# Performance work log

Hardware: AMD Instinct MI355X
Metric: run time of the kernel (lower is better)

Reference implementation:

```python
import jax, jax.numpy as jnp
import numpy as np

B, S, DIN, PPOS = 2, 128, 768, 256
DCAT = 2 * (DIN + PPOS)   # 2048, BiLSTM input dim
H = DCAT // 2             # 1024, LSTM hidden per direction
MAXLEN = 128              # position embedding table size


def _xavier(k, shape):
    lim = float(np.sqrt(6.0 / (shape[0] + shape[1])))
    return jax.random.uniform(k, shape, jnp.float32, -lim, lim)


def _lstm_u(k, shape):
    lim = float(1.0 / np.sqrt(H))
    return jax.random.uniform(k, shape, jnp.float32, -lim, lim)


def setup_inputs() -> dict:
    key = jax.random.key(0)
    ks = jax.random.split(key, 17)
    inp = {
        "input_embeddings": jax.random.normal(ks[0], (B, S, DIN), jnp.float32),
        "pos_emb": _xavier(ks[1], (MAXLEN, PPOS)),
    }
    i = 2
    for l in (0, 1):
        for d in ("f", "b"):
            inp[f"w_ih_l{l}_{d}"] = _lstm_u(ks[i], (4 * H, DCAT)); i += 1
            inp[f"b_ih_l{l}_{d}"] = _lstm_u(ks[i], (4 * H,)); i += 1
            inp[f"b_hh_l{l}_{d}"] = _lstm_u(ks[i], (4 * H,)); i += 1
    inp["fc_w"] = _lstm_u(ks[i], (1, 2 * H)); i += 1
    inp["fc_b"] = _lstm_u(ks[i], (1,))
    inp["convo_len"] = S
    return inp


def _lstm_dir(x, w_ih, b_ih, b_hh):
    # single timestep, h0=c0=0 -> recurrent term vanishes (grad wrt W_hh is 0)
    g = x @ w_ih.T + b_ih + b_hh            # [N, 4H], pytorch gate order i,f,g,o
    i, f, c, o = jnp.split(g, 4, axis=-1)
    cell = jax.nn.sigmoid(i) * jnp.tanh(c)  # f-gate multiplies c0=0
    return jax.nn.sigmoid(o) * jnp.tanh(cell)


def reference(input_embeddings, pos_emb,
              w_ih_l0_f, b_ih_l0_f, b_hh_l0_f,
              w_ih_l0_b, b_ih_l0_b, b_hh_l0_b,
              w_ih_l1_f, b_ih_l1_f, b_hh_l1_f,
              w_ih_l1_b, b_ih_l1_b, b_hh_l1_b,
              fc_w, fc_b, convo_len):
    # positions indexed by int(norm(embedding)) as in the original code
    idx = jnp.linalg.norm(input_embeddings, axis=-1).astype(jnp.int32)  # [B,S]
    e = jnp.concatenate([input_embeddings, pos_emb[idx]], axis=-1)      # [B,S,D']
    # pair (i,j) -> concat(e_i, e_j)
    left = jnp.repeat(e, S, axis=1)          # [B, S*S, D'], row i repeated S times
    right = jnp.tile(e, (1, S, 1))           # [B, S*S, D'], sequence tiled S times
    p = jnp.concatenate([left, right], axis=-1).reshape(B * S * S, DCAT)
    h1 = jnp.concatenate([
        _lstm_dir(p, w_ih_l0_f, b_ih_l0_f, b_hh_l0_f),
        _lstm_dir(p, w_ih_l0_b, b_ih_l0_b, b_hh_l0_b)], axis=-1)        # [N, 2H]
    h2 = jnp.concatenate([
        _lstm_dir(h1, w_ih_l1_f, b_ih_l1_f, b_hh_l1_f),
        _lstm_dir(h1, w_ih_l1_b, b_ih_l1_b, b_hh_l1_b)], axis=-1)       # [N, 2H]
    logits = h2 @ fc_w.T + fc_b              # [N, 1]
    return logits.reshape(B, S * S)
```

## Files before the change

kernel.cpp:

```cpp
#include <hip/hip_runtime.h>
#include <cstdint>

typedef _Float16 f16;
typedef f16   f16x8 __attribute__((ext_vector_type(8)));
typedef f16   f16x4 __attribute__((ext_vector_type(4)));
typedef float f32x4 __attribute__((ext_vector_type(4)));
typedef float f32x8 __attribute__((ext_vector_type(8)));
typedef int   i32x4 __attribute__((ext_vector_type(4)));
typedef signed char c8x8 __attribute__((ext_vector_type(8)));
typedef unsigned int u32;


static constexpr size_t OFF_E16  = 0;
static constexpr size_t OFF_W0P  = 524288;
static constexpr size_t OFF_UV   = 34078720;
static constexpr size_t OFF_B0   = 50855936;
static constexpr size_t OFF_W1P  = 50888704;
static constexpr size_t OFF_B1   = 76054528;
static constexpr size_t OFF_H1   = 76079104;
static constexpr size_t OFF_PART = 210296832;

__device__ __forceinline__ void gl_lds16(const void* g, void* l) {
  __builtin_amdgcn_global_load_lds((const __attribute__((address_space(1))) u32*)g,
                                   (__attribute__((address_space(3))) u32*)l, 16, 0, 0);
}
__device__ __forceinline__ float sigm(float x) { return 1.f / (1.f + __expf(-x)); }
__device__ __forceinline__ float tanh_f(float x) {
  float e = __expf(-2.f * fabsf(x));
  float t = (1.f - e) / (1.f + e);
  return x < 0.f ? -t : t;
}


__global__ __launch_bounds__(256) void prep_e(const float* __restrict__ x,
                                              const float* __restrict__ pos,
                                              f16* __restrict__ e16) {
  int row = blockIdx.x;
  const float* xr = x + (size_t)row * 768;
  double ss = 0.0;
  for (int i = threadIdx.x; i < 768; i += 256) { float v = xr[i]; ss += (double)v * v; }
  __shared__ double red[256];
  red[threadIdx.x] = ss;
  __syncthreads();
  for (int s2 = 128; s2 > 0; s2 >>= 1) {
    if (threadIdx.x < s2) red[threadIdx.x] += red[threadIdx.x + s2];
    __syncthreads();
  }
  __shared__ int idx_s;
  if (threadIdx.x == 0) {
    int idx = (int)((float)sqrt(red[0]));
    idx_s = idx < 0 ? 0 : (idx > 127 ? 127 : idx);
  }
  __syncthreads();
  int idx = idx_s;
  for (int i = threadIdx.x; i < 1024; i += 256) {
    float v = (i < 768) ? xr[i] : pos[idx * 256 + (i - 768)];
    e16[(size_t)row * 1024 + i] = (f16)v;
  }
}

__global__ __launch_bounds__(256) void prep_w0(const float* __restrict__ w0f,
                                               const float* __restrict__ w0b,
                                               f16* __restrict__ w0p) {
  int t = blockIdx.x * 256 + threadIdx.x;
  int n = t >> 8;
  int k4 = (t & 255) * 4;
  int half = n >> 13;
  int nn = n & 8191;
  int d = nn >> 12;
  int r = nn & 4095;
  const float* w = d ? w0b : w0f;
  float4 v = *(const float4*)(w + (size_t)r * 2048 + half * 1024 + k4);
  f16x4 o;
  o[0] = (f16)v.x; o[1] = (f16)v.y; o[2] = (f16)v.z; o[3] = (f16)v.w;
  *(f16x4*)(w0p + (size_t)n * 1024 + k4) = o;
}

__global__ __launch_bounds__(256) void prep_w1(const float* __restrict__ w1f,
                                               const float* __restrict__ w1b,
                                               signed char* __restrict__ w1q) {
  int t = blockIdx.x * 256 + threadIdx.x;
  int n = t >> 8;
  int c8 = (t & 255) * 8;
  int ct = n / 192, r = n % 192;
  int wn = r / 48, r2 = r % 48;
  int g = r2 >> 4, hs = r2 & 15;
  int d = ct >> 4;
  int h = (ct & 15) * 64 + wn * 16 + hs;
  int gsel = (g == 0) ? 0 : (g + 1);
  const float* w = d ? w1b : w1f;
  const float* src = w + (size_t)(gsel * 1024 + h) * 2048 + c8;
  float4 v0 = *(const float4*)(src);
  float4 v1 = *(const float4*)(src + 4);
  c8x8 o;
  o[0] = (signed char)(int)rintf(v0.x * 4064.f);
  o[1] = (signed char)(int)rintf(v0.y * 4064.f);
  o[2] = (signed char)(int)rintf(v0.z * 4064.f);
  o[3] = (signed char)(int)rintf(v0.w * 4064.f);
  o[4] = (signed char)(int)rintf(v1.x * 4064.f);
  o[5] = (signed char)(int)rintf(v1.y * 4064.f);
  o[6] = (signed char)(int)rintf(v1.z * 4064.f);
  o[7] = (signed char)(int)rintf(v1.w * 4064.f);
  *(c8x8*)(w1q + (size_t)n * 2048 + c8) = o;
}

__global__ void prep_bias(const float* bi0f, const float* bh0f,
                          const float* bi0b, const float* bh0b,
                          const float* bi1f, const float* bh1f,
                          const float* bi1b, const float* bh1b,
                          float* bias0, float* bias1) {
  int i = blockIdx.x * 256 + threadIdx.x;
  if (i < 8192) {
    int d = i >> 12, r = i & 4095;
    bias0[i] = d ? (bi0b[r] + bh0b[r]) : (bi0f[r] + bh0f[r]);
  } else if (i < 8192 + 6144) {
    int n = i - 8192;
    int d = n / 3072, rem = n % 3072;
    int g3 = rem >> 10, k = rem & 1023;
    int gsel = (g3 == 0) ? 0 : (g3 + 1);
    int r = gsel * 1024 + k;
    bias1[n] = d ? (bi1b[r] + bh1b[r]) : (bi1f[r] + bh1f[r]);
  }
}

__global__ __launch_bounds__(256) void gemm_l0(const f16* __restrict__ e16,
                                               const f16* __restrict__ w0p,
                                               float* __restrict__ uv) {
  __shared__ __align__(16) f16 As[8192];
  __shared__ __align__(16) f16 Bs[8192];
  int n0 = blockIdx.x * 128;
  int m0 = blockIdx.y * 128;
  int tid = threadIdx.x, lane = tid & 63, w = tid >> 6;
  int wr = (w >> 1) * 64, wc = (w & 1) * 64;
  f32x4 acc[4][4] = {};

  for (int k0 = 0; k0 < 1024; k0 += 64) {
    __syncthreads();
#pragma unroll
    for (int q = 0; q < 4; q++) {
      int ch = tid + q * 256;
      int c = ch >> 7, r = ch & 127;
      gl_lds16(e16 + (size_t)(m0 + r) * 1024 + k0 + c * 8, (char*)As + ch * 16);
    }
#pragma unroll
    for (int q = 0; q < 4; q++) {
      int ch = tid + q * 256;
      int c = ch >> 7, r = ch & 127;
      gl_lds16(w0p + (size_t)(n0 + r) * 1024 + k0 + c * 8, (char*)Bs + ch * 16);
    }
    __syncthreads();
#pragma unroll
    for (int ks = 0; ks < 2; ks++) {
      int cb = ks * 4 + (lane >> 4);
      f16x8 a[4], b[4];
#pragma unroll
      for (int f = 0; f < 4; f++)
        a[f] = *(const f16x8*)(As + (cb * 128 + wr + f * 16 + (lane & 15)) * 8);
#pragma unroll
      for (int g = 0; g < 4; g++)
        b[g] = *(const f16x8*)(Bs + (cb * 128 + wc + g * 16 + (lane & 15)) * 8);
#pragma unroll
      for (int f = 0; f < 4; f++)
#pragma unroll
        for (int g = 0; g < 4; g++)
          acc[f][g] = __builtin_amdgcn_mfma_f32_16x16x32_f16(a[f], b[g], acc[f][g], 0, 0, 0);
    }
  }
  int col = lane & 15, lg = lane >> 4;
#pragma unroll
  for (int f = 0; f < 4; f++)
#pragma unroll
    for (int g = 0; g < 4; g++)
#pragma unroll
      for (int j = 0; j < 4; j++) {
        int row = m0 + wr + f * 16 + lg * 4 + j;
        int c = n0 + wc + g * 16 + col;
        uv[(size_t)row * 16384 + c] = acc[f][g][j];
      }
}

__global__ __launch_bounds__(256) void pair_h1(const float* __restrict__ uv,
                                               const float* __restrict__ bias0,
                                               signed char* __restrict__ h1q) {
  int row = blockIdx.x;
  int urow = row >> 7;
  int b = row >> 14;
  int vrow = (b << 7) | (row & 127);
  int t = threadIdx.x;
  int u = t * 8;
  int d = u >> 10, k = u & 1023;
  const float* ub = uv + (size_t)urow * 16384 + d * 4096 + k;
  const float* vb = uv + (size_t)vrow * 16384 + 8192 + d * 4096 + k;
  const float* bb = bias0 + d * 4096 + k;
  f32x8 ui = *(const f32x8*)(ub);
  f32x8 uc = *(const f32x8*)(ub + 2048);
  f32x8 uo = *(const f32x8*)(ub + 3072);
  f32x8 vi = *(const f32x8*)(vb);
  f32x8 vc = *(const f32x8*)(vb + 2048);
  f32x8 vo = *(const f32x8*)(vb + 3072);
  f32x8 bi = *(const f32x8*)(bb);
  f32x8 bc = *(const f32x8*)(bb + 2048);
  f32x8 bo = *(const f32x8*)(bb + 3072);
  c8x8 ov;
#pragma unroll
  for (int e = 0; e < 8; e++) {
    float gi = ui[e] + vi[e] + bi[e];
    float gc = uc[e] + vc[e] + bc[e];
    float go = uo[e] + vo[e] + bo[e];
    float cell = sigm(gi) * tanh_f(gc);
    float hv = sigm(go) * tanh_f(cell);
    ov[e] = (signed char)(int)rintf(hv * 127.f);
  }
  *(c8x8*)(h1q + (size_t)row * 2048 + u) = ov;
}

__global__ __launch_bounds__(256, 2) void gemm_l1(const signed char* __restrict__ h1q,
                                                  const signed char* __restrict__ w1q,
                                                  const float* __restrict__ bias1,
                                                  const float* __restrict__ fcw,
                                                  float* __restrict__ partial) {
  __shared__ __align__(16) signed char As[2][16384];
  __shared__ __align__(16) signed char Bs[2][24576];
  int ct = blockIdx.x;
  int m0 = blockIdx.y * 128;
  int d = ct >> 4;
  int tid = threadIdx.x, lane = tid & 63;
  int wn = tid >> 6;
  int la = lane & 15, lq = lane >> 4, l8 = lane & 7;

  const signed char* asrc[4]; signed char* adst[4];
#pragma unroll
  for (int q = 0; q < 4; q++) {
    int ch = tid + q * 256, r = ch >> 3, slot = ch & 7, c = slot ^ (r & 7);
    asrc[q] = h1q + (size_t)(m0 + r) * 2048 + c * 16;
    adst[q] = &As[0][ch * 16];
  }
  const signed char* bsrc[6]; signed char* bdst[6];
#pragma unroll
  for (int q = 0; q < 6; q++) {
    int ch = tid + q * 256, pr = ch >> 3, slot = ch & 7, c = slot ^ (pr & 7);
    bsrc[q] = w1q + (size_t)(ct * 192 + pr) * 2048 + c * 16;
    bdst[q] = &Bs[0][ch * 16];
  }
  auto stage = [&](int t, int b) {
#pragma unroll
    for (int q = 0; q < 4; q++) gl_lds16(asrc[q] + t * 128, adst[q] + b * 16384);
#pragma unroll
    for (int q = 0; q < 6; q++) gl_lds16(bsrc[q] + t * 128, bdst[q] + b * 24576);
  };

  i32x4 acc[8][3] = {};
  stage(0, 0);
  stage(1, 1);
  asm volatile("s_waitcnt vmcnt(10)" ::: "memory");
  __builtin_amdgcn_s_barrier();

  for (int t = 0; t < 16; ++t) {
    int b = t & 1;
    const signed char* Ab = &As[b][0];
    const signed char* Bb = &Bs[b][0];
    i32x4 af[2][8], bf[2][3];
#pragma unroll
    for (int ks = 0; ks < 2; ks++) {
      int slot = (ks * 4 + lq) ^ l8;
#pragma unroll
      for (int rf = 0; rf < 8; rf++)
        af[ks][rf] = *(const i32x4*)(Ab + ((rf * 16 + la) * 8 + slot) * 16);
#pragma unroll
      for (int cf = 0; cf < 3; cf++)
        bf[ks][cf] = *(const i32x4*)(Bb + ((wn * 48 + cf * 16 + la) * 8 + slot) * 16);
    }
    __builtin_amdgcn_s_setprio(1);
#pragma unroll
    for (int rf = 0; rf < 8; rf++)
#pragma unroll
      for (int cf = 0; cf < 3; cf++)
        acc[rf][cf] = __builtin_amdgcn_mfma_i32_16x16x64_i8(af[0][rf], bf[0][cf], acc[rf][cf], 0, 0, 0);
    __builtin_amdgcn_s_setprio(0);
    asm volatile("s_waitcnt lgkmcnt(0)" ::: "memory");
    __builtin_amdgcn_sched_barrier(0);
    __builtin_amdgcn_s_barrier();
    if (t < 14) stage(t + 2, b);
    __builtin_amdgcn_s_setprio(1);
#pragma unroll
    for (int rf = 0; rf < 8; rf++)
#pragma unroll
      for (int cf = 0; cf < 3; cf++)
        acc[rf][cf] = __builtin_amdgcn_mfma_i32_16x16x64_i8(af[1][rf], bf[1][cf], acc[rf][cf], 0, 0, 0);
    __builtin_amdgcn_s_setprio(0);
    if (t < 14)      { asm volatile("s_waitcnt vmcnt(10)" ::: "memory"); }
    else if (t == 14){ asm volatile("s_waitcnt vmcnt(0)"  ::: "memory"); }
    __builtin_amdgcn_s_barrier();
  }

  float* sred = (float*)&As[0][0];
  const float S = 1.0f / 516128.0f;
  int hcol = (ct & 15) * 64 + wn * 16 + la;
  float bi = bias1[(d * 3 + 0) * 1024 + hcol];
  float bc = bias1[(d * 3 + 1) * 1024 + hcol];
  float bo = bias1[(d * 3 + 2) * 1024 + hcol];
  float wf = fcw[d * 1024 + hcol];
#pragma unroll
  for (int rf = 0; rf < 8; rf++) {
#pragma unroll
    for (int j = 0; j < 4; j++) {
      float gi = (float)acc[rf][0][j] * S + bi;
      float gc = (float)acc[rf][1][j] * S + bc;
      float go = (float)acc[rf][2][j] * S + bo;
      float cell = sigm(gi) * tanh_f(gc);
      float hv = sigm(go) * tanh_f(cell);
      float v = hv * wf;
      v += __shfl_xor(v, 1);
      v += __shfl_xor(v, 2);
      v += __shfl_xor(v, 4);
      v += __shfl_xor(v, 8);
      if (la == 0) sred[wn * 128 + rf * 16 + lq * 4 + j] = v;
    }
  }
  __syncthreads();
  if (tid < 128) {
    float s = sred[tid] + sred[128 + tid] + sred[256 + tid] + sred[384 + tid];
    partial[(size_t)ct * 32768 + m0 + tid] = s;
  }
}

__global__ void reduce_out(const float* __restrict__ partial,
                           const float* __restrict__ fcb,
                           float* __restrict__ out) {
  int m = blockIdx.x * 256 + threadIdx.x;
  float s = fcb[0];
#pragma unroll
  for (int ct = 0; ct < 32; ct++) s += partial[(size_t)ct * 32768 + m];
  out[m] = s;
}

extern "C" void kernel_launch(void* const* d_in, const int* in_sizes, int n_in,
                              void* d_out, int out_size, void* d_ws, size_t ws_size,
                              hipStream_t stream) {
  const float* x    = (const float*)d_in[0];
  const float* pos  = (const float*)d_in[1];
  const float* w0f  = (const float*)d_in[2];
  const float* bi0f = (const float*)d_in[3];
  const float* bh0f = (const float*)d_in[4];
  const float* w0b  = (const float*)d_in[5];
  const float* bi0b = (const float*)d_in[6];
  const float* bh0b = (const float*)d_in[7];
  const float* w1f  = (const float*)d_in[8];
  const float* bi1f = (const float*)d_in[9];
  const float* bh1f = (const float*)d_in[10];
  const float* w1b  = (const float*)d_in[11];
  const float* bi1b = (const float*)d_in[12];
  const float* bh1b = (const float*)d_in[13];
  const float* fcw  = (const float*)d_in[14];
  const float* fcb  = (const float*)d_in[15];
  float* out = (float*)d_out;

  char* ws = (char*)d_ws;
  f16*   e16   = (f16*)(ws + OFF_E16);
  f16*   w0p   = (f16*)(ws + OFF_W0P);
  float* uv    = (float*)(ws + OFF_UV);
  float* bias0 = (float*)(ws + OFF_B0);
  signed char* w1q = (signed char*)(ws + OFF_W1P);
  float* bias1 = (float*)(ws + OFF_B1);
  signed char* h1q = (signed char*)(ws + OFF_H1);
  float* part  = (float*)(ws + OFF_PART);

  prep_e<<<256, 256, 0, stream>>>(x, pos, e16);
  prep_w0<<<16384, 256, 0, stream>>>(w0f, w0b, w0p);
  prep_w1<<<6144, 256, 0, stream>>>(w1f, w1b, w1q);
  prep_bias<<<56, 256, 0, stream>>>(bi0f, bh0f, bi0b, bh0b, bi1f, bh1f, bi1b, bh1b,
                                    bias0, bias1);
  gemm_l0<<<dim3(128, 2), 256, 0, stream>>>(e16, w0p, uv);
  pair_h1<<<32768, 256, 0, stream>>>(uv, bias0, h1q);
  gemm_l1<<<dim3(32, 256), 256, 0, stream>>>(h1q, w1q, bias1, fcw, part);
  reduce_out<<<128, 256, 0, stream>>>(part, fcb, out);
}
```

Before: 722.2 us.

## Enlarge layer-1 GEMM tile to 256 rows with 8 waves and interleaved staging

The int8 layer-1 GEMM block now covers 256 rows by 192 weight columns using 512 threads arranged as 2x4 waves, so each weight tile loaded into LDS serves twice as many rows. The K loop is split into four sub-phases, and the next tile's A and B global-to-LDS copies are issued during the first two, in a double-buffered pipeline. The grid is reordered so consecutive blocks share the same weight column tile. The cost is more barriers per K step, a larger LDS footprint (112KB per block) and possibly lower occupancy.

Result: slower. 795.0 us (+10.1%).

```diff
diff --git a/kernel.cpp b/kernel.cpp
--- a/kernel.cpp
+++ b/kernel.cpp
@@ -214,83 +214,92 @@
   *(c8x8*)(h1q + (size_t)row * 2048 + u) = ov;
 }
 
-__global__ __launch_bounds__(256, 2) void gemm_l1(const signed char* __restrict__ h1q,
+__global__ __launch_bounds__(512, 2) void gemm_l1(const signed char* __restrict__ h1q,
                                                   const signed char* __restrict__ w1q,
                                                   const float* __restrict__ bias1,
                                                   const float* __restrict__ fcw,
                                                   float* __restrict__ partial) {
-  __shared__ __align__(16) signed char As[2][16384];
+  __shared__ __align__(16) signed char As[2][32768];
   __shared__ __align__(16) signed char Bs[2][24576];
-  int ct = blockIdx.x;
-  int m0 = blockIdx.y * 128;
+  int m0 = blockIdx.x * 256;
+  int ct = blockIdx.y;
   int d = ct >> 4;
-  int tid = threadIdx.x, lane = tid & 63;
-  int wn = tid >> 6;
+  int tid = threadIdx.x, lane = tid & 63, w = tid >> 6;
+  int wm = w >> 2, wn = w & 3;
   int la = lane & 15, lq = lane >> 4, l8 = lane & 7;
 
   const signed char* asrc[4]; signed char* adst[4];
 #pragma unroll
   for (int q = 0; q < 4; q++) {
-    int ch = tid + q * 256, r = ch >> 3, slot = ch & 7, c = slot ^ (r & 7);
+    int ch = tid + q * 512, r = ch >> 3, slot = ch & 7, c = slot ^ (r & 7);
     asrc[q] = h1q + (size_t)(m0 + r) * 2048 + c * 16;
     adst[q] = &As[0][ch * 16];
   }
-  const signed char* bsrc[6]; signed char* bdst[6];
-#pragma unroll
-  for (int q = 0; q < 6; q++) {
-    int ch = tid + q * 256, pr = ch >> 3, slot = ch & 7, c = slot ^ (pr & 7);
+  const signed char* bsrc[3]; signed char* bdst[3];
+#pragma unroll
+  for (int q = 0; q < 3; q++) {
+    int ch = tid + q * 512, pr = ch >> 3, slot = ch & 7, c = slot ^ (pr & 7);
     bsrc[q] = w1q + (size_t)(ct * 192 + pr) * 2048 + c * 16;
     bdst[q] = &Bs[0][ch * 16];
   }
-  auto stage = [&](int t, int b) {
-#pragma unroll
-    for (int q = 0; q < 4; q++) gl_lds16(asrc[q] + t * 128, adst[q] + b * 16384);
-#pragma unroll
-    for (int q = 0; q < 6; q++) gl_lds16(bsrc[q] + t * 128, bdst[q] + b * 24576);
+  auto stageA = [&](int t, int b) {
+#pragma unroll
+    for (int q = 0; q < 4; q++) gl_lds16(asrc[q] + t * 128, adst[q] + b * 32768);
   };
+  auto stageB = [&](int t, int b) {
+#pragma unroll
+    for (int q = 0; q < 3; q++) gl_lds16(bsrc[q] + t * 128, bdst[q] + b * 24576);
+  };
 
   i32x4 acc[8][3] = {};
-  stage(0, 0);
-  stage(1, 1);
-  asm volatile("s_waitcnt vmcnt(10)" ::: "memory");
+  stageA(0, 0); stageB(0, 0);
+  asm volatile("s_waitcnt vmcnt(0)" ::: "memory");
   __builtin_amdgcn_s_barrier();
 
   for (int t = 0; t < 16; ++t) {
     int b = t & 1;
     const signed char* Ab = &As[b][0];
     const signed char* Bb = &Bs[b][0];
-    i32x4 af[2][8], bf[2][3];
-#pragma unroll
-    for (int ks = 0; ks < 2; ks++) {
-      int slot = (ks * 4 + lq) ^ l8;
-#pragma unroll
-      for (int rf = 0; rf < 8; rf++)
-        af[ks][rf] = *(const i32x4*)(Ab + ((rf * 16 + la) * 8 + slot) * 16);
-#pragma unroll
-      for (int cf = 0; cf < 3; cf++)
-        bf[ks][cf] = *(const i32x4*)(Bb + ((wn * 48 + cf * 16 + la) * 8 + slot) * 16);
-    }
-    __builtin_amdgcn_s_setprio(1);
-#pragma unroll
-    for (int rf = 0; rf < 8; rf++)
-#pragma unroll
-      for (int cf = 0; cf < 3; cf++)
-        acc[rf][cf] = __builtin_amdgcn_mfma_i32_16x16x64_i8(af[0][rf], bf[0][cf], acc[rf][cf], 0, 0, 0);
-    __builtin_amdgcn_s_setprio(0);
-    asm volatile("s_waitcnt lgkmcnt(0)" ::: "memory");
-    __builtin_amdgcn_sched_barrier(0);
-    __builtin_amdgcn_s_barrier();
-    if (t < 14) stage(t + 2, b);
-    __builtin_amdgcn_s_setprio(1);
-#pragma unroll
-    for (int rf = 0; rf < 8; rf++)
-#pragma unroll
-      for (int cf = 0; cf < 3; cf++)
-        acc[rf][cf] = __builtin_amdgcn_mfma_i32_16x16x64_i8(af[1][rf], bf[1][cf], acc[rf][cf], 0, 0, 0);
-    __builtin_amdgcn_s_setprio(0);
-    if (t < 14)      { asm volatile("s_waitcnt vmcnt(10)" ::: "memory"); }
-    else if (t == 14){ asm volatile("s_waitcnt vmcnt(0)"  ::: "memory"); }
-    __builtin_amdgcn_s_barrier();
+    i32x4 bf[2][3];
+#pragma unroll
+    for (int p = 0; p < 4; p++) {
+      i32x4 a[2][2];
+#pragma unroll
+      for (int ks = 0; ks < 2; ks++) {
+        int slot = (ks * 4 + lq) ^ l8;
+#pragma unroll
+        for (int rq = 0; rq < 2; rq++) {
+          int R = wm * 128 + (p * 2 + rq) * 16 + la;
+          a[ks][rq] = *(const i32x4*)(Ab + (R * 8 + slot) * 16);
+        }
+        if (p == 0) {
+#pragma unroll
+          for (int cf = 0; cf < 3; cf++) {
+            int P = wn * 48 + cf * 16 + la;
+            bf[ks][cf] = *(const i32x4*)(Bb + (P * 8 + slot) * 16);
+          }
+        }
+      }
+      if (t < 15) {
+        if (p == 0) stageA(t + 1, b ^ 1);
+        else if (p == 1) stageB(t + 1, b ^ 1);
+      }
+      __builtin_amdgcn_s_barrier();
+      asm volatile("s_waitcnt lgkmcnt(0)" ::: "memory");
+      __builtin_amdgcn_sched_barrier(0);
+      __builtin_amdgcn_s_setprio(1);
+#pragma unroll
+      for (int ks = 0; ks < 2; ks++)
+#pragma unroll
+        for (int rq = 0; rq < 2; rq++)
+#pragma unroll
+          for (int cf = 0; cf < 3; cf++)
+            acc[p * 2 + rq][cf] = __builtin_amdgcn_mfma_i32_16x16x64_i8(
+                a[ks][rq], bf[ks][cf], acc[p * 2 + rq][cf], 0, 0, 0);
+      __builtin_amdgcn_s_setprio(0);
+      if (p == 3 && t < 15) { asm volatile("s_waitcnt vmcnt(0)" ::: "memory"); }
+      __builtin_amdgcn_s_barrier();
+    }
   }
 
   float* sred = (float*)&As[0][0];
@@ -314,12 +323,12 @@
       v += __shfl_xor(v, 2);
       v += __shfl_xor(v, 4);
       v += __shfl_xor(v, 8);
-      if (la == 0) sred[wn * 128 + rf * 16 + lq * 4 + j] = v;
+      if (la == 0) sred[wn * 256 + wm * 128 + rf * 16 + lq * 4 + j] = v;
     }
   }
   __syncthreads();
-  if (tid < 128) {
-    float s = sred[tid] + sred[128 + tid] + sred[256 + tid] + sred[384 + tid];
+  if (tid < 256) {
+    float s = sred[tid] + sred[256 + tid] + sred[512 + tid] + sred[768 + tid];
     partial[(size_t)ct * 32768 + m0 + tid] = s;
   }
 }
@@ -372,6 +381,6 @@
                                     bias0, bias1);
   gemm_l0<<<dim3(128, 2), 256, 0, stream>>>(e16, w0p, uv);
   pair_h1<<<32768, 256, 0, stream>>>(uv, bias0, h1q);
-  gemm_l1<<<dim3(32, 256), 256, 0, stream>>>(h1q, w1q, bias1, fcw, part);
+  gemm_l1<<<dim3(128, 32), 512, 0, stream>>>(h1q, w1q, bias1, fcw, part);
   reduce_out<<<128, 256, 0, stream>>>(part, fcb, out);
 }
```

## Load A fragments directly from global and triple-buffer B tiles in LDS

Applied to the files above, without the earlier changes.

The layer-1 GEMM no longer stages the activation (A) tile through shared memory. Each wave now reads its A fragments straight from global memory into registers, and only the weight (B) tile still goes through LDS, now with a three-deep buffer ring and one barrier per k-step instead of two. This is meant to cut LDS traffic and barrier overhead, and LDS use per block drops. In exchange every one of the four waves loads the same A data redundantly from global or L2, and those loads sit on the critical path with little latency hiding.

After: 1.362 ms. +88.7%, slower.

```diff
diff --git a/kernel.cpp b/kernel.cpp
--- a/kernel.cpp
+++ b/kernel.cpp
@@ -219,8 +219,7 @@
                                                   const float* __restrict__ bias1,
                                                   const float* __restrict__ fcw,
                                                   float* __restrict__ partial) {
-  __shared__ __align__(16) signed char As[2][16384];
-  __shared__ __align__(16) signed char Bs[2][24576];
+  __shared__ __align__(16) signed char Bs[3][24576];
   int ct = blockIdx.x;
   int m0 = blockIdx.y * 128;
   int d = ct >> 4;
@@ -228,13 +227,6 @@
   int wn = tid >> 6;
   int la = lane & 15, lq = lane >> 4, l8 = lane & 7;
 
-  const signed char* asrc[4]; signed char* adst[4];
-#pragma unroll
-  for (int q = 0; q < 4; q++) {
-    int ch = tid + q * 256, r = ch >> 3, slot = ch & 7, c = slot ^ (r & 7);
-    asrc[q] = h1q + (size_t)(m0 + r) * 2048 + c * 16;
-    adst[q] = &As[0][ch * 16];
-  }
   const signed char* bsrc[6]; signed char* bdst[6];
 #pragma unroll
   for (int q = 0; q < 6; q++) {
@@ -242,58 +234,55 @@
     bsrc[q] = w1q + (size_t)(ct * 192 + pr) * 2048 + c * 16;
     bdst[q] = &Bs[0][ch * 16];
   }
-  auto stage = [&](int t, int b) {
-#pragma unroll
-    for (int q = 0; q < 4; q++) gl_lds16(asrc[q] + t * 128, adst[q] + b * 16384);
-#pragma unroll
-    for (int q = 0; q < 6; q++) gl_lds16(bsrc[q] + t * 128, bdst[q] + b * 24576);
+  auto stageB = [&](int t, int sb) {
+#pragma unroll
+    for (int q = 0; q < 6; q++) gl_lds16(bsrc[q] + t * 128, bdst[q] + sb * 24576);
   };
 
+  const signed char* abase = h1q + (size_t)(m0 + la) * 2048 + lq * 16;
+
   i32x4 acc[8][3] = {};
-  stage(0, 0);
-  stage(1, 1);
-  asm volatile("s_waitcnt vmcnt(10)" ::: "memory");
+  stageB(0, 0);
+  stageB(1, 1);
+  asm volatile("s_waitcnt vmcnt(0)" ::: "memory");
   __builtin_amdgcn_s_barrier();
 
   for (int t = 0; t < 16; ++t) {
-    int b = t & 1;
-    const signed char* Ab = &As[b][0];
-    const signed char* Bb = &Bs[b][0];
-    i32x4 af[2][8], bf[2][3];
+    int buf = t % 3;
+    int sb = buf + 2; if (sb >= 3) sb -= 3;
+    const signed char* Bb = &Bs[buf][0];
+    i32x4 af[2][8];
+#pragma unroll
+    for (int ks = 0; ks < 2; ks++)
+#pragma unroll
+      for (int rf = 0; rf < 8; rf++)
+        af[ks][rf] = *(const i32x4*)(abase + (size_t)rf * 32768 + t * 128 + ks * 64);
+    if (t < 14) stageB(t + 2, sb);
+    i32x4 bf[2][3];
 #pragma unroll
     for (int ks = 0; ks < 2; ks++) {
       int slot = (ks * 4 + lq) ^ l8;
 #pragma unroll
-      for (int rf = 0; rf < 8; rf++)
-        af[ks][rf] = *(const i32x4*)(Ab + ((rf * 16 + la) * 8 + slot) * 16);
-#pragma unroll
       for (int cf = 0; cf < 3; cf++)
         bf[ks][cf] = *(const i32x4*)(Bb + ((wn * 48 + cf * 16 + la) * 8 + slot) * 16);
     }
     __builtin_amdgcn_s_setprio(1);
 #pragma unroll
-    for (int rf = 0; rf < 8; rf++)
-#pragma unroll
-      for (int cf = 0; cf < 3; cf++)
-        acc[rf][cf] = __builtin_amdgcn_mfma_i32_16x16x64_i8(af[0][rf], bf[0][cf], acc[rf][cf], 0, 0, 0);
+    for (int ks = 0; ks < 2; ks++)
+#pragma unroll
+      for (int rf = 0; rf < 8; rf++)
+#pragma unroll
+        for (int cf = 0; cf < 3; cf++)
+          acc[rf][cf] = __builtin_amdgcn_mfma_i32_16x16x64_i8(
+              af[ks][rf], bf[ks][cf], acc[rf][cf], 0, 0, 0);
     __builtin_amdgcn_s_setprio(0);
-    asm volatile("s_waitcnt lgkmcnt(0)" ::: "memory");
+    if (t < 14)      { asm volatile("s_waitcnt vmcnt(6)" ::: "memory"); }
+    else             { asm volatile("s_waitcnt vmcnt(0)" ::: "memory"); }
     __builtin_amdgcn_sched_barrier(0);
     __builtin_amdgcn_s_barrier();
-    if (t < 14) stage(t + 2, b);
-    __builtin_amdgcn_s_setprio(1);
-#pragma unroll
-    for (int rf = 0; rf < 8; rf++)
-#pragma unroll
-      for (int cf = 0; cf < 3; cf++)
-        acc[rf][cf] = __builtin_amdgcn_mfma_i32_16x16x64_i8(af[1][rf], bf[1][cf], acc[rf][cf], 0, 0, 0);
-    __builtin_amdgcn_s_setprio(0);
-    if (t < 14)      { asm volatile("s_waitcnt vmcnt(10)" ::: "memory"); }
-    else if (t == 14){ asm volatile("s_waitcnt vmcnt(0)"  ::: "memory"); }
-    __builtin_amdgcn_s_barrier();
-  }
-
-  float* sred = (float*)&As[0][0];
+  }
+
+  float* sred = (float*)&Bs[0][0];
   const float S = 1.0f / 516128.0f;
   int hcol = (ct & 15) * 64 + wn * 16 + la;
   float bi = bias1[(d * 3 + 0) * 1024 + hcol];
```
